# Kernel optimization log

Hardware: AMD Instinct MI355X
Metric: run time of the kernel (lower is better)

Reference implementation:

```python
import jax, jax.numpy as jnp
import numpy as np
from jax import lax

B, Hm, Wm, C, HEADS, MLP_H = 16, 56, 56, 256, 4, 1024
N = Hm * Wm
GRID_STRIDE = 4
N_GRID = (Hm // GRID_STRIDE) * (Wm // GRID_STRIDE)  # 196
K_DOWN = N // 4                                      # 784
K_ADA = K_DOWN - N_GRID
H2, W2 = Hm // 2, Wm // 2
POOL = 7


def _token_order():
    # get_loc: grid tokens first, then adaptive tokens
    pos = np.arange(N)
    tmp = pos.reshape(Hm, Wm)
    pos_grid = tmp[GRID_STRIDE // 2::GRID_STRIDE, GRID_STRIDE // 2::GRID_STRIDE].reshape(-1)
    m = np.ones(N, bool)
    m[pos_grid] = False
    return np.concatenate([pos_grid, pos[m]])


def _loc_init():
    y = 2.0 * ((np.arange(Hm) + 0.5) / Hm) - 1.0
    x = 2.0 * ((np.arange(Wm) + 0.5) / Wm) - 1.0
    xm, ym = np.meshgrid(x, y)
    return np.stack([xm, ym], -1).reshape(-1, 2).astype(np.float32)


_ORDER = _token_order()
_LOC = _loc_init()[_ORDER]


def _ln(x, g, b, eps=1e-5):
    m = jnp.mean(x, -1, keepdims=True)
    v = jnp.mean((x - m) ** 2, -1, keepdims=True)
    return (x - m) * lax.rsqrt(v + eps) * g + b


def _gauss_kernel(ks=3, sigma=2.0):
    c = np.arange(ks, dtype=np.float32)
    xg = np.tile(c, ks).reshape(ks, ks)
    yg = xg.T
    mean = (ks - 1) / 2.0
    var = sigma ** 2
    k = np.exp(-((xg - mean) ** 2 + (yg - mean) ** 2) / (2 * var)) / (2 * np.pi * var)
    return (k / k.sum()).astype(np.float32)


def _gauss_filt(x):
    ch = x.shape[1]
    w = jnp.broadcast_to(jnp.asarray(_gauss_kernel())[None, None], (ch, 1, 3, 3))
    return lax.conv_general_dilated(x, w, (1, 1), [(1, 1), (1, 1)],
                                    feature_group_count=ch,
                                    dimension_numbers=('NCHW', 'OIHW', 'NCHW'))


def _token2map(x, loc, H, W):
    # scatter-add tokens into a [H,W] map, average by count, gaussian hole-fill
    b, n, c = x.shape
    loc = jnp.clip(loc, -1, 1)
    px = jnp.clip(jnp.round(0.5 * (loc[..., 0] + 1) * W - 0.5).astype(jnp.int32), 0, W - 1)
    py = jnp.clip(jnp.round(0.5 * (loc[..., 1] + 1) * H - 0.5).astype(jnp.int32), 0, H - 1)
    idx = (px + py * W + jnp.arange(b)[:, None] * H * W).reshape(-1)
    src = jnp.concatenate([x, jnp.ones((b, n, 1), x.dtype)], -1).reshape(b * n, c + 1)
    out = jnp.zeros((b * H * W, c + 1), x.dtype).at[idx].add(src)
    out = out.reshape(b, H, W, c + 1).transpose(0, 3, 1, 2)
    feat, mask = out[:, :c], out[:, c:]
    feat = feat / (mask + 1e-6)
    mask = (mask > 0).astype(x.dtype)
    feat = feat * mask
    # reconstruct_feature (kernel_size=3, sigma=2)
    fm = _gauss_filt(jnp.concatenate([feat, mask], 1))
    fi = fm[:, :c] / (fm[:, c:] + 1e-6)
    mi = (fm[:, c:] > 0).astype(x.dtype)
    fi = fi * mi
    return feat + (1 - mask) * fi


def _map2token(fm, loc):
    # bilinear grid_sample, align_corners=False, zeros padding
    b, c, H, W = fm.shape
    x = (loc[..., 0] + 1) * 0.5 * W - 0.5
    y = (loc[..., 1] + 1) * 0.5 * H - 0.5
    x0 = jnp.floor(x)
    y0 = jnp.floor(y)
    wx = x - x0
    wy = y - y0
    fm_flat = fm.reshape(b, c, H * W)

    def gather(xi, yi):
        valid = ((xi >= 0) & (xi < W) & (yi >= 0) & (yi < H)).astype(fm.dtype)
        ii = (jnp.clip(yi, 0, H - 1) * W + jnp.clip(xi, 0, W - 1)).astype(jnp.int32)
        v = jnp.take_along_axis(fm_flat, ii[:, None, :], axis=2)  # [b,c,k]
        return v * valid[:, None, :]

    x0i = x0.astype(jnp.int32)
    y0i = y0.astype(jnp.int32)
    v00 = gather(x0i, y0i)
    v01 = gather(x0i + 1, y0i)
    v10 = gather(x0i, y0i + 1)
    v11 = gather(x0i + 1, y0i + 1)
    wx = wx[:, None, :]
    wy = wy[:, None, :]
    out = (v00 * (1 - wx) * (1 - wy) + v01 * wx * (1 - wy)
           + v10 * (1 - wx) * wy + v11 * wx * wy)
    return out.transpose(0, 2, 1)  # [b,k,c]


def _forward(x, ln1_g, ln1_b, wq, wkv, wproj, bproj, sr_w, sr_b, srn_g, srn_b,
             ln2_g, ln2_b, fc1_w, fc1_b, dw_w, dw_b, fc2_w, fc2_b, conf_w, conf_b):
    order = jnp.asarray(_ORDER)
    x = jnp.take(x, order, axis=1)                       # get_loc reorder
    loc = jnp.broadcast_to(jnp.asarray(_LOC)[None], (B, N, 2))
    d = C // HEADS
    # ---- PVT attention (spatial-reduction via 7x7 adaptive pool + 1x1 conv)
    xn = _ln(x, ln1_g, ln1_b)
    q = (xn @ wq).reshape(B, N, HEADS, d).transpose(0, 2, 1, 3)
    fmap = xn.transpose(0, 2, 1).reshape(B, C, Hm, Wm)
    pooled = fmap.reshape(B, C, POOL, Hm // POOL, POOL, Wm // POOL).mean((3, 5))
    sr = jnp.einsum('bihw,oi->bohw', pooled, sr_w) + sr_b[None, :, None, None]
    t = sr.reshape(B, C, POOL * POOL).transpose(0, 2, 1)
    t = jax.nn.gelu(_ln(t, srn_g, srn_b), approximate=False)
    kv = (t @ wkv).reshape(B, POOL * POOL, 2, HEADS, d)
    k = kv[:, :, 0].transpose(0, 2, 1, 3)
    v = kv[:, :, 1].transpose(0, 2, 1, 3)
    a = jax.nn.softmax(jnp.einsum('bhnd,bhmd->bhnm', q, k) * (d ** -0.5), axis=-1)
    o = jnp.einsum('bhnm,bhmd->bhnd', a, v).transpose(0, 2, 1, 3).reshape(B, N, C)
    x = x + o @ wproj + bproj
    # ---- MLP with depthwise conv
    xn = _ln(x, ln2_g, ln2_b)
    h = jax.nn.relu(xn @ fc1_w + fc1_b)
    hm = h.transpose(0, 2, 1).reshape(B, MLP_H, Hm, Wm)
    hm = lax.conv_general_dilated(hm, dw_w, (1, 1), [(1, 1), (1, 1)],
                                  feature_group_count=MLP_H,
                                  dimension_numbers=('NCHW', 'OIHW', 'NCHW'))
    hm = hm + dw_b[None, :, None, None]
    h = jax.nn.gelu(hm.reshape(B, MLP_H, N).transpose(0, 2, 1), approximate=False)
    x = x + h @ fc2_w + fc2_b
    # ---- gumbel top-k selection among adaptive tokens (grid tokens kept)
    conf = (x @ conf_w + conf_b)[..., 0]                 # [B,N]
    u = jax.random.uniform(jax.random.key(1), (B, N - N_GRID), x.dtype)
    g = -jnp.log(-jnp.log(u + 1e-6) + 1e-6)
    scores = conf[:, N_GRID:] + g                        # T=1
    _, idx = lax.top_k(scores, K_ADA)
    x_ada = jnp.take_along_axis(x[:, N_GRID:], idx[..., None], axis=1)
    loc_ada = jnp.take_along_axis(loc[:, N_GRID:], idx[..., None], axis=1)
    x_down = jnp.concatenate([x[:, :N_GRID], x_ada], 1)      # [B,784,C]
    loc_down = jnp.concatenate([loc[:, :N_GRID], loc_ada], 1)
    # ---- token2map (scatter-add + gaussian fill) then map2token (grid sample)
    fmap2 = _token2map(x, loc, H2, W2)
    tok = _map2token(fmap2, loc_down)
    return x_down + tok


def setup_inputs() -> dict:
    key = jax.random.key(0)
    ks = jax.random.split(key, 10)
    s = 0.02

    def rn(k, shape):
        return jax.random.normal(k, shape, jnp.float32) * s

    return {
        'x': jax.random.normal(ks[0], (B, N, C), jnp.float32),
        'ln1_g': jnp.ones((C,), jnp.float32), 'ln1_b': jnp.zeros((C,), jnp.float32),
        'wq': rn(ks[1], (C, C)), 'wkv': rn(ks[2], (C, 2 * C)),
        'wproj': rn(ks[3], (C, C)), 'bproj': jnp.zeros((C,), jnp.float32),
        'sr_w': rn(ks[4], (C, C)), 'sr_b': jnp.zeros((C,), jnp.float32),
        'srn_g': jnp.ones((C,), jnp.float32), 'srn_b': jnp.zeros((C,), jnp.float32),
        'ln2_g': jnp.ones((C,), jnp.float32), 'ln2_b': jnp.zeros((C,), jnp.float32),
        'fc1_w': rn(ks[5], (C, MLP_H)), 'fc1_b': jnp.zeros((MLP_H,), jnp.float32),
        'dw_w': rn(ks[6], (MLP_H, 1, 3, 3)), 'dw_b': jnp.zeros((MLP_H,), jnp.float32),
        'fc2_w': rn(ks[7], (MLP_H, C)), 'fc2_b': jnp.zeros((C,), jnp.float32),
        'conf_w': rn(ks[8], (C, 1)), 'conf_b': jnp.zeros((1,), jnp.float32),
    }


def reference(x, ln1_g, ln1_b, wq, wkv, wproj, bproj, sr_w, sr_b, srn_g, srn_b,
              ln2_g, ln2_b, fc1_w, fc1_b, dw_w, dw_b, fc2_w, fc2_b, conf_w, conf_b):
    return _forward(x, ln1_g, ln1_b, wq, wkv, wproj, bproj, sr_w, sr_b, srn_g, srn_b,
                    ln2_g, ln2_b, fc1_w, fc1_b, dw_w, dw_b, fc2_w, fc2_b, conf_w, conf_b)
```

## Files before the change

### kernel.cpp

```cpp
#include <hip/hip_runtime.h>
#include <math.h>


#define BB 16
#define NN 3136
#define CC 256
#define NHEADS 4
#define DH 64
#define MLPH 1024
#define NGRID 196
#define NREST 2940
#define KADA 588
#define HW 56
#define BCH 2

__device__ __forceinline__ int inv_order(int p) {
  int r = p / HW, c = p % HW;
  if ((r & 3) == 2 && (c & 3) == 2) return (r >> 2) * 14 + (c >> 2);
  int g = ((r + 1) >> 2) * 14 + (((r & 3) == 2) ? ((c + 1) >> 2) : 0);
  return NGRID + p - g;
}

__device__ __forceinline__ double gelu_d(double v) {
  return 0.5 * v * (1.0 + erf(v * 0.70710678118654752440));
}

__device__ __forceinline__ void tf2x32k(unsigned k0, unsigned k1, unsigned x0, unsigned x1,
                                        unsigned& o0, unsigned& o1) {
  unsigned ks[3] = {k0, k1, k0 ^ k1 ^ 0x1BD11BDAu};
  x0 += ks[0]; x1 += ks[1];
  const int rot[2][4] = {{13,15,26,6},{17,29,16,24}};
  #pragma unroll
  for (int i = 0; i < 5; ++i) {
    #pragma unroll
    for (int j = 0; j < 4; ++j) {
      int rr = rot[i & 1][j];
      x0 += x1;
      x1 = (x1 << rr) | (x1 >> (32 - rr));
      x1 ^= x0;
    }
    x0 += ks[(i + 1) % 3];
    x1 += ks[(i + 2) % 3] + (unsigned)(i + 1);
  }
  o0 = x0; o1 = x1;
}

__device__ bool tf_kat() {
  unsigned a, b;
  tf2x32k(0u, 0u, 0u, 0u, a, b);
  if (a != 0x6b200159u || b != 0x99ba4efeu) return false;
  tf2x32k(0xffffffffu, 0xffffffffu, 0xffffffffu, 0xffffffffu, a, b);
  if (a != 0x1cb996fcu || b != 0xbb002be7u) return false;
  tf2x32k(0x13198a2eu, 0x03707344u, 0x243f6a88u, 0x85a308d3u, a, b);
  if (a != 0xc4923a9cu || b != 0x483df7a0u) return false;
  return true;
}

__device__ __forceinline__ double gumbel_d(int f) {
  unsigned o0, o1;
  tf2x32k(0u, 1u, 0u, (unsigned)f, o0, o1);
  unsigned bits = o0 ^ o1;
  float u = __uint_as_float((bits >> 9) | 0x3f800000u) - 1.0f;
  double ud = (double)u;
  return -log(-log(ud + 1e-6) + 1e-6);
}

__global__ void k_order(int* __restrict__ ord) {
  int p = blockIdx.x * 256 + threadIdx.x;
  if (p < NN) ord[inv_order(p)] = p;
}

__global__ __launch_bounds__(256) void k_ln1(const float* __restrict__ x,
    const float* __restrict__ g, const float* __restrict__ b2,
    float* __restrict__ x_r, float* __restrict__ xn) {
  int b = blockIdx.x / NN, p = blockIdx.x % NN;
  int t = threadIdx.x;
  __shared__ double red[256];
  float v = x[((size_t)b*NN + p)*CC + t];
  double vd = (double)v;
  red[t] = vd; __syncthreads();
  for (int s = 128; s > 0; s >>= 1) { if (t < s) red[t] += red[t+s]; __syncthreads(); }
  double m = red[0] * (1.0/CC);
  __syncthreads();
  double d = vd - m;
  red[t] = d*d; __syncthreads();
  for (int s = 128; s > 0; s >>= 1) { if (t < s) red[t] += red[t+s]; __syncthreads(); }
  double var = red[0] * (1.0/CC);
  double o = d * (1.0 / sqrt(var + 1e-5)) * (double)g[t] + (double)b2[t];
  int n = inv_order(p);
  size_t dst = ((size_t)b*NN + n)*CC + t;
  x_r[dst] = v;
  xn[dst] = (float)o;
}

__global__ __launch_bounds__(256) void k_ln2(const float* __restrict__ xin,
    const float* __restrict__ g, const float* __restrict__ b2, float* __restrict__ xo) {
  int row = blockIdx.x;
  int t = threadIdx.x;
  __shared__ double red[256];
  double v = (double)xin[(size_t)row*CC + t];
  red[t] = v; __syncthreads();
  for (int s = 128; s > 0; s >>= 1) { if (t < s) red[t] += red[t+s]; __syncthreads(); }
  double m = red[0] * (1.0/CC);
  __syncthreads();
  double d = v - m;
  red[t] = d*d; __syncthreads();
  for (int s = 128; s > 0; s >>= 1) { if (t < s) red[t] += red[t+s]; __syncthreads(); }
  double var = red[0] * (1.0/CC);
  xo[(size_t)row*CC + t] = (float)(d * (1.0 / sqrt(var + 1e-5)) * (double)g[t] + (double)b2[t]);
}

__global__ __launch_bounds__(256) void k_sr(const float* __restrict__ xn,
    const float* __restrict__ sr_w, const float* __restrict__ sr_b, float* __restrict__ srout) {
  int b = blockIdx.x / 49, cell = blockIdx.x % 49;
  int p1 = cell / 7, p2 = cell % 7;
  int t = threadIdx.x;
  __shared__ double pl[256];
  double s = 0.0;
  #pragma unroll
  for (int i = 0; i < 8; ++i)
    #pragma unroll
    for (int j = 0; j < 8; ++j) {
      int n = (p1*8 + i)*HW + (p2*8 + j);
      s += (double)xn[((size_t)b*NN + n)*CC + t];
    }
  pl[t] = s * (1.0/64.0);
  __syncthreads();
  double acc = (double)sr_b[t];
  for (int i = 0; i < CC; ++i) acc += pl[i] * (double)sr_w[t*CC + i];
  srout[((size_t)b*49 + cell)*CC + t] = (float)acc;
}

__global__ __launch_bounds__(256) void k_kv(const float* __restrict__ srout,
    const float* __restrict__ g, const float* __restrict__ b2,
    const float* __restrict__ wkv, float* __restrict__ kb, float* __restrict__ vb) {
  int b = blockIdx.x / 49, m = blockIdx.x % 49;
  int t = threadIdx.x;
  __shared__ double red[256];
  __shared__ double tl[256];
  double v = (double)srout[((size_t)b*49 + m)*CC + t];
  red[t] = v; __syncthreads();
  for (int s = 128; s > 0; s >>= 1) { if (t < s) red[t] += red[t+s]; __syncthreads(); }
  double mean = red[0] * (1.0/CC);
  __syncthreads();
  double d = v - mean;
  red[t] = d*d; __syncthreads();
  for (int s = 128; s > 0; s >>= 1) { if (t < s) red[t] += red[t+s]; __syncthreads(); }
  double var = red[0] * (1.0/CC);
  double o = d * (1.0 / sqrt(var + 1e-5)) * (double)g[t] + (double)b2[t];
  tl[t] = gelu_d(o);
  __syncthreads();
  #pragma unroll
  for (int rep = 0; rep < 2; ++rep) {
    int j = t + rep*256;
    double acc = 0.0;
    for (int i = 0; i < CC; ++i) acc += tl[i] * (double)wkv[(size_t)i*512 + j];
    int h = (j >> 6) & 3, dd = j & 63;
    float* dst = (j >> 8) ? vb : kb;
    dst[(((size_t)b*NHEADS + h)*49 + m)*DH + dd] = (float)acc;
  }
}

template<int BIAS, int RELU, int RESID>
__global__ __launch_bounds__(256) void k_gemm64(const float* __restrict__ A,
    const float* __restrict__ Bw, const float* __restrict__ bias,
    const float* resid, float* Co, int M, int N, int K) {
  __shared__ __align__(16) float As[16][68];
  __shared__ __align__(16) float Bs[16][68];
  int tid = threadIdx.x;
  int n0 = blockIdx.x * 64, m0 = blockIdx.y * 64;
  int tx = tid & 15, ty = tid >> 4;
  int aM = tid >> 2, aK = (tid & 3) * 4;
  int bK = tid >> 4, bN = (tid & 15) * 4;
  double acc[4][4] = {};
  for (int k0 = 0; k0 < K; k0 += 16) {
    float4 a4 = *(const float4*)&A[(size_t)(m0 + aM) * K + k0 + aK];
    As[aK+0][aM] = a4.x; As[aK+1][aM] = a4.y; As[aK+2][aM] = a4.z; As[aK+3][aM] = a4.w;
    float4 b4 = *(const float4*)&Bw[(size_t)(k0 + bK) * N + n0 + bN];
    *(float4*)&Bs[bK][bN] = b4;
    __syncthreads();
    #pragma unroll
    for (int k = 0; k < 16; ++k) {
      double av[4], bv[4];
      #pragma unroll
      for (int r = 0; r < 4; ++r) av[r] = (double)As[k][ty*4 + r];
      #pragma unroll
      for (int c = 0; c < 4; ++c) bv[c] = (double)Bs[k][tx*4 + c];
      #pragma unroll
      for (int r = 0; r < 4; ++r)
        #pragma unroll
        for (int c = 0; c < 4; ++c)
          acc[r][c] = fma(av[r], bv[c], acc[r][c]);
    }
    __syncthreads();
  }
  #pragma unroll
  for (int r = 0; r < 4; ++r) {
    size_t off = (size_t)(m0 + ty*4 + r) * N + n0 + tx*4;
    #pragma unroll
    for (int c = 0; c < 4; ++c) {
      double v = acc[r][c];
      if (BIAS)  v += (double)bias[n0 + tx*4 + c];
      if (RESID) v += (double)resid[off + c];
      if (RELU)  v = fmax(v, 0.0);
      Co[off + c] = (float)v;
    }
  }
}

__global__ __launch_bounds__(64) void k_attn(float* __restrict__ q,
    const float* __restrict__ kb, const float* __restrict__ vb) {
  int b = blockIdx.x / NN, n = blockIdx.x % NN;
  int t = threadIdx.x;
  __shared__ float qs[256];
  __shared__ double lg[4][52];
  __shared__ double sinv[4];
  float* qrow = q + ((size_t)b*NN + n)*CC;
  #pragma unroll
  for (int i = 0; i < 4; ++i) qs[t + i*64] = qrow[t + i*64];
  __syncthreads();
  for (int li = t; li < 196; li += 64) {
    int h = li / 49, m = li % 49;
    const float* kr = kb + (((size_t)b*NHEADS + h)*49 + m)*DH;
    const float* qh = qs + h*DH;
    double acc = 0.0;
    #pragma unroll 16
    for (int d = 0; d < DH; ++d) acc = fma((double)qh[d], (double)kr[d], acc);
    lg[h][m] = acc * 0.125;
  }
  __syncthreads();
  if (t < 4) {
    double mx = -1e300;
    for (int j = 0; j < 49; ++j) mx = fmax(mx, lg[t][j]);
    double s = 0.0;
    for (int j = 0; j < 49; ++j) { double e = exp(lg[t][j] - mx); lg[t][j] = e; s += e; }
    sinv[t] = 1.0 / s;
  }
  __syncthreads();
  #pragma unroll
  for (int h = 0; h < 4; ++h) {
    const float* vr = vb + (((size_t)b*NHEADS + h)*49)*DH + t;
    double acc = 0.0;
    for (int m = 0; m < 49; ++m) acc = fma(lg[h][m], (double)vr[m*DH], acc);
    qrow[h*64 + t] = (float)(acc * sinv[h]);
  }
}

__global__ __launch_bounds__(256) void k_dw(const float* __restrict__ hb,
    const float* __restrict__ w, const float* __restrict__ bias, float* __restrict__ h2) {
  int bl = blockIdx.x / NN, n = blockIdx.x % NN;
  int r = n / HW, c = n % HW;
  int t = threadIdx.x;
  const size_t base = (size_t)bl * NN;
  #pragma unroll
  for (int it = 0; it < 4; ++it) {
    int mc = t + it*256;
    double acc = (double)bias[mc];
    #pragma unroll
    for (int ky = 0; ky < 3; ++ky) {
      int rr = r + ky - 1;
      if (rr < 0 || rr >= HW) continue;
      #pragma unroll
      for (int kx = 0; kx < 3; ++kx) {
        int cc2 = c + kx - 1;
        if (cc2 < 0 || cc2 >= HW) continue;
        acc = fma((double)w[mc*9 + ky*3 + kx], (double)hb[(base + rr*HW + cc2)*MLPH + mc], acc);
      }
    }
    h2[(base + n)*MLPH + mc] = (float)gelu_d(acc);
  }
}

__global__ __launch_bounds__(1024) void k_topk(const float* __restrict__ x3,
    const float* __restrict__ cw, const float* __restrict__ cb, int* __restrict__ sel) {
  int b = blockIdx.x, t = threadIdx.x;
  __shared__ float wsm[256];
  __shared__ double sc[NREST];
  if (t < 256) wsm[t] = cw[t];
  __syncthreads();
  for (int i = t; i < NREST; i += 1024) {
    const float* xr = x3 + ((size_t)b*NN + NGRID + i)*CC;
    double acc = (double)cb[0];
    #pragma unroll 8
    for (int c = 0; c < CC; ++c) acc += (double)xr[c] * (double)wsm[c];
    sc[i] = acc + gumbel_d(b*NREST + i);
  }
  __syncthreads();
  for (int i = t; i < NREST; i += 1024) {
    double si = sc[i];
    int rank = 0;
    for (int j = 0; j < NREST; ++j) {
      double sj = sc[j];
      rank += (int)((sj > si) | ((sj == si) & (j < i)));
    }
    if (rank < KADA) sel[b*KADA + rank] = NGRID + i;
  }
}

__global__ __launch_bounds__(256) void k_t2m(const float* __restrict__ x3, float* __restrict__ fm) {
  int b = blockIdx.x / 784, pix = blockIdx.x % 784;
  int py = pix / 28, px = pix % 28;
  int t = threadIdx.x;
  float s = 0.f;
  #pragma unroll
  for (int dy = 0; dy < 2; ++dy)
    #pragma unroll
    for (int dx = 0; dx < 2; ++dx) {
      int p = (2*py + dy)*HW + 2*px + dx;
      s += x3[((size_t)b*NN + inv_order(p))*CC + t];
    }
  fm[((size_t)b*784 + pix)*CC + t] = s * (1.0f / 4.000001f);
}

__global__ __launch_bounds__(256) void k_out(const float* __restrict__ x3,
    const float* __restrict__ fm, const int* __restrict__ sel,
    const int* __restrict__ ord, float* __restrict__ out) {
  int b = blockIdx.x / 784, slot = blockIdx.x % 784;
  int t = threadIdx.x;
  int n = (slot < NGRID) ? slot : sel[b*KADA + slot - NGRID];
  int p = ord[n];
  int r = p / HW, c = p % HW;
  int ix0 = (c - 1) >> 1;
  int iy0 = (r - 1) >> 1;
  float wx = (c & 1) ? 0.25f : 0.75f;
  float wy = (r & 1) ? 0.25f : 0.75f;
  const float* fb = fm + (size_t)b*784*CC + t;
  float v = 0.f;
  float w00 = (1.f-wx)*(1.f-wy), w01 = wx*(1.f-wy), w10 = (1.f-wx)*wy, w11 = wx*wy;
  if (ix0 >= 0   && iy0 >= 0)   v += w00 * fb[(iy0*28 + ix0)*CC];
  if (ix0+1 < 28 && iy0 >= 0)   v += w01 * fb[(iy0*28 + ix0+1)*CC];
  if (ix0 >= 0   && iy0+1 < 28) v += w10 * fb[((iy0+1)*28 + ix0)*CC];
  if (ix0+1 < 28 && iy0+1 < 28) v += w11 * fb[((iy0+1)*28 + ix0+1)*CC];
  float res = x3[((size_t)b*NN + n)*CC + t] + v;
  if (blockIdx.x == 0 && t == 0) {
    if (!tf_kat()) res += 1000.0f;
  }
  out[((size_t)b*784 + slot)*CC + t] = res;
}

extern "C" void kernel_launch(void* const* d_in, const int* in_sizes, int n_in,
                              void* d_out, int out_size, void* d_ws, size_t ws_size,
                              hipStream_t stream) {
  const float* x      = (const float*)d_in[0];
  const float* ln1_g  = (const float*)d_in[1];
  const float* ln1_b  = (const float*)d_in[2];
  const float* wq     = (const float*)d_in[3];
  const float* wkv    = (const float*)d_in[4];
  const float* wproj  = (const float*)d_in[5];
  const float* bproj  = (const float*)d_in[6];
  const float* sr_w   = (const float*)d_in[7];
  const float* sr_b   = (const float*)d_in[8];
  const float* srn_g  = (const float*)d_in[9];
  const float* srn_b  = (const float*)d_in[10];
  const float* ln2_g  = (const float*)d_in[11];
  const float* ln2_b  = (const float*)d_in[12];
  const float* fc1_w  = (const float*)d_in[13];
  const float* fc1_b  = (const float*)d_in[14];
  const float* dw_w   = (const float*)d_in[15];
  const float* dw_b   = (const float*)d_in[16];
  const float* fc2_w  = (const float*)d_in[17];
  const float* fc2_b  = (const float*)d_in[18];
  const float* conf_w = (const float*)d_in[19];
  const float* conf_b = (const float*)d_in[20];
  float* out = (float*)d_out;

  float* ws = (float*)d_ws;
  const size_t SZ_XN = (size_t)BB*NN*CC;
  const size_t SZ_H  = (size_t)BCH*NN*MLPH;
  float* x_r   = ws;
  float* xn    = x_r + SZ_XN;
  float* qbuf  = xn + SZ_XN;
  float* hb    = qbuf + SZ_XN;
  float* h2b   = hb + SZ_H;
  float* srout = h2b + SZ_H;
  float* kb    = srout + (size_t)BB*49*CC;
  float* vb    = kb + (size_t)BB*NHEADS*49*DH;
  float* fm    = vb + (size_t)BB*NHEADS*49*DH;
  int*   sel   = (int*)(fm + (size_t)BB*784*CC);
  int*   ord   = sel + BB*KADA;

  k_order<<<(NN+255)/256, 256, 0, stream>>>(ord);
  k_ln1<<<BB*NN, 256, 0, stream>>>(x, ln1_g, ln1_b, x_r, xn);
  k_sr<<<BB*49, 256, 0, stream>>>(xn, sr_w, sr_b, srout);
  k_kv<<<BB*49, 256, 0, stream>>>(srout, srn_g, srn_b, wkv, kb, vb);
  k_gemm64<0,0,0><<<dim3(CC/64, BB*NN/64), 256, 0, stream>>>(xn, wq, nullptr, nullptr, qbuf, BB*NN, CC, CC);
  k_attn<<<BB*NN, 64, 0, stream>>>(qbuf, kb, vb);
  k_gemm64<1,0,1><<<dim3(CC/64, BB*NN/64), 256, 0, stream>>>(qbuf, wproj, bproj, x_r, x_r, BB*NN, CC, CC);
  k_ln2<<<BB*NN, 256, 0, stream>>>(x_r, ln2_g, ln2_b, xn);
  for (int bc = 0; bc < BB/BCH; ++bc) {
    const size_t ro = (size_t)bc * BCH * NN;
    k_gemm64<1,1,0><<<dim3(MLPH/64, BCH*NN/64), 256, 0, stream>>>(xn + ro*CC, fc1_w, fc1_b, nullptr, hb, BCH*NN, MLPH, CC);
    k_dw<<<BCH*NN, 256, 0, stream>>>(hb, dw_w, dw_b, h2b);
    k_gemm64<1,0,1><<<dim3(CC/64, BCH*NN/64), 256, 0, stream>>>(h2b, fc2_w, fc2_b, x_r + ro*CC, x_r + ro*CC, BCH*NN, CC, MLPH);
  }
  k_topk<<<BB, 1024, 0, stream>>>(x_r, conf_w, conf_b, sel);
  k_t2m<<<BB*784, 256, 0, stream>>>(x_r, fm);
  k_out<<<BB*784, 256, 0, stream>>>(x_r, fm, sel, ord, out);
}
```

Before: 3.859 ms.

## Use wave-shuffle LayerNorm reductions, 128-row GEMM tiles, and split top-k into parallel kernels

Replaces the shared-memory tree reductions in the three LayerNorm kernels with 64-lane shuffle reductions and a four-slot combine, cutting barriers. Adds a 128x64 GEMM variant with 8x4 per-thread outputs for the Q, projection and fc1 GEMMs, keeping the 64x64 kernel for fc2. Splits the top-k into a wave-per-token confidence kernel and a ranking kernel spread across 6 blocks per batch, where the old version ran only 16 blocks. Larger GEMM tiles raise register pressure and halve the block count, and the shuffle reductions sum in a different order, so low-order bits can change.

```diff
diff --git a/kernel.cpp b/kernel.cpp
--- a/kernel.cpp
+++ b/kernel.cpp
@@ -75,38 +75,48 @@
     float* __restrict__ x_r, float* __restrict__ xn) {
   int b = blockIdx.x / NN, p = blockIdx.x % NN;
   int t = threadIdx.x;
-  __shared__ double red[256];
+  __shared__ double la[4], lb[4];
   float v = x[((size_t)b*NN + p)*CC + t];
   double vd = (double)v;
-  red[t] = vd; __syncthreads();
-  for (int s = 128; s > 0; s >>= 1) { if (t < s) red[t] += red[t+s]; __syncthreads(); }
-  double m = red[0] * (1.0/CC);
-  __syncthreads();
+  double s = vd;
+  #pragma unroll
+  for (int o = 32; o; o >>= 1) s += __shfl_xor(s, o, 64);
+  if ((t & 63) == 0) la[t >> 6] = s;
+  __syncthreads();
+  double m = (la[0] + la[1] + la[2] + la[3]) * (1.0/CC);
   double d = vd - m;
-  red[t] = d*d; __syncthreads();
-  for (int s = 128; s > 0; s >>= 1) { if (t < s) red[t] += red[t+s]; __syncthreads(); }
-  double var = red[0] * (1.0/CC);
-  double o = d * (1.0 / sqrt(var + 1e-5)) * (double)g[t] + (double)b2[t];
+  s = d * d;
+  #pragma unroll
+  for (int o = 32; o; o >>= 1) s += __shfl_xor(s, o, 64);
+  if ((t & 63) == 0) lb[t >> 6] = s;
+  __syncthreads();
+  double var = (lb[0] + lb[1] + lb[2] + lb[3]) * (1.0/CC);
+  double o2 = d * (1.0 / sqrt(var + 1e-5)) * (double)g[t] + (double)b2[t];
   int n = inv_order(p);
   size_t dst = ((size_t)b*NN + n)*CC + t;
   x_r[dst] = v;
-  xn[dst] = (float)o;
+  xn[dst] = (float)o2;
 }
 
 __global__ __launch_bounds__(256) void k_ln2(const float* __restrict__ xin,
     const float* __restrict__ g, const float* __restrict__ b2, float* __restrict__ xo) {
   int row = blockIdx.x;
   int t = threadIdx.x;
-  __shared__ double red[256];
+  __shared__ double la[4], lb[4];
   double v = (double)xin[(size_t)row*CC + t];
-  red[t] = v; __syncthreads();
-  for (int s = 128; s > 0; s >>= 1) { if (t < s) red[t] += red[t+s]; __syncthreads(); }
-  double m = red[0] * (1.0/CC);
-  __syncthreads();
+  double s = v;
+  #pragma unroll
+  for (int o = 32; o; o >>= 1) s += __shfl_xor(s, o, 64);
+  if ((t & 63) == 0) la[t >> 6] = s;
+  __syncthreads();
+  double m = (la[0] + la[1] + la[2] + la[3]) * (1.0/CC);
   double d = v - m;
-  red[t] = d*d; __syncthreads();
-  for (int s = 128; s > 0; s >>= 1) { if (t < s) red[t] += red[t+s]; __syncthreads(); }
-  double var = red[0] * (1.0/CC);
+  s = d * d;
+  #pragma unroll
+  for (int o = 32; o; o >>= 1) s += __shfl_xor(s, o, 64);
+  if ((t & 63) == 0) lb[t >> 6] = s;
+  __syncthreads();
+  double var = (lb[0] + lb[1] + lb[2] + lb[3]) * (1.0/CC);
   xo[(size_t)row*CC + t] = (float)(d * (1.0 / sqrt(var + 1e-5)) * (double)g[t] + (double)b2[t]);
 }
 
@@ -136,19 +146,24 @@
     const float* __restrict__ wkv, float* __restrict__ kb, float* __restrict__ vb) {
   int b = blockIdx.x / 49, m = blockIdx.x % 49;
   int t = threadIdx.x;
-  __shared__ double red[256];
+  __shared__ double la[4], lb[4];
   __shared__ double tl[256];
   double v = (double)srout[((size_t)b*49 + m)*CC + t];
-  red[t] = v; __syncthreads();
-  for (int s = 128; s > 0; s >>= 1) { if (t < s) red[t] += red[t+s]; __syncthreads(); }
-  double mean = red[0] * (1.0/CC);
-  __syncthreads();
+  double s = v;
+  #pragma unroll
+  for (int o = 32; o; o >>= 1) s += __shfl_xor(s, o, 64);
+  if ((t & 63) == 0) la[t >> 6] = s;
+  __syncthreads();
+  double mean = (la[0] + la[1] + la[2] + la[3]) * (1.0/CC);
   double d = v - mean;
-  red[t] = d*d; __syncthreads();
-  for (int s = 128; s > 0; s >>= 1) { if (t < s) red[t] += red[t+s]; __syncthreads(); }
-  double var = red[0] * (1.0/CC);
-  double o = d * (1.0 / sqrt(var + 1e-5)) * (double)g[t] + (double)b2[t];
-  tl[t] = gelu_d(o);
+  s = d * d;
+  #pragma unroll
+  for (int o = 32; o; o >>= 1) s += __shfl_xor(s, o, 64);
+  if ((t & 63) == 0) lb[t >> 6] = s;
+  __syncthreads();
+  double var = (lb[0] + lb[1] + lb[2] + lb[3]) * (1.0/CC);
+  double o2 = d * (1.0 / sqrt(var + 1e-5)) * (double)g[t] + (double)b2[t];
+  tl[t] = gelu_d(o2);
   __syncthreads();
   #pragma unroll
   for (int rep = 0; rep < 2; ++rep) {
@@ -162,7 +177,58 @@
 }
 
 template<int BIAS, int RELU, int RESID>
-__global__ __launch_bounds__(256) void k_gemm64(const float* __restrict__ A,
+__global__ __launch_bounds__(256) void k_gemmA(const float* __restrict__ A,
+    const float* __restrict__ Bw, const float* __restrict__ bias,
+    const float* resid, float* Co, int M, int N, int K) {
+  __shared__ __align__(16) float As[16][132];
+  __shared__ __align__(16) float Bs[16][68];
+  int tid = threadIdx.x;
+  int n0 = blockIdx.x * 64, m0 = blockIdx.y * 128;
+  int tx = tid & 15, ty = tid >> 4;
+  int aM = tid >> 2, aK = (tid & 3) * 4;
+  int bK = tid >> 4, bN = (tid & 15) * 4;
+  double acc[8][4] = {};
+  for (int k0 = 0; k0 < K; k0 += 16) {
+    #pragma unroll
+    for (int ps = 0; ps < 2; ++ps) {
+      float4 a4 = *(const float4*)&A[(size_t)(m0 + aM + ps*64) * K + k0 + aK];
+      As[aK+0][aM+ps*64] = a4.x; As[aK+1][aM+ps*64] = a4.y;
+      As[aK+2][aM+ps*64] = a4.z; As[aK+3][aM+ps*64] = a4.w;
+    }
+    float4 b4 = *(const float4*)&Bw[(size_t)(k0 + bK) * N + n0 + bN];
+    *(float4*)&Bs[bK][bN] = b4;
+    __syncthreads();
+    #pragma unroll
+    for (int k = 0; k < 16; ++k) {
+      double av[8], bv[4];
+      #pragma unroll
+      for (int r = 0; r < 8; ++r) av[r] = (double)As[k][ty*8 + r];
+      #pragma unroll
+      for (int c = 0; c < 4; ++c) bv[c] = (double)Bs[k][tx*4 + c];
+      #pragma unroll
+      for (int r = 0; r < 8; ++r)
+        #pragma unroll
+        for (int c = 0; c < 4; ++c)
+          acc[r][c] = fma(av[r], bv[c], acc[r][c]);
+    }
+    __syncthreads();
+  }
+  #pragma unroll
+  for (int r = 0; r < 8; ++r) {
+    size_t off = (size_t)(m0 + ty*8 + r) * N + n0 + tx*4;
+    #pragma unroll
+    for (int c = 0; c < 4; ++c) {
+      double v = acc[r][c];
+      if (BIAS)  v += (double)bias[n0 + tx*4 + c];
+      if (RESID) v += (double)resid[off + c];
+      if (RELU)  v = fmax(v, 0.0);
+      Co[off + c] = (float)v;
+    }
+  }
+}
+
+template<int BIAS, int RELU, int RESID>
+__global__ __launch_bounds__(256) void k_gemmB(const float* __restrict__ A,
     const float* __restrict__ Bw, const float* __restrict__ bias,
     const float* resid, float* Co, int M, int N, int K) {
   __shared__ __align__(16) float As[16][68];
@@ -271,24 +337,33 @@
   }
 }
 
-__global__ __launch_bounds__(1024) void k_topk(const float* __restrict__ x3,
-    const float* __restrict__ cw, const float* __restrict__ cb, int* __restrict__ sel) {
-  int b = blockIdx.x, t = threadIdx.x;
-  __shared__ float wsm[256];
+__global__ __launch_bounds__(256) void k_conf(const float* __restrict__ x3,
+    const float* __restrict__ cw, const float* __restrict__ cb, double* __restrict__ scd) {
+  int wid = (blockIdx.x * 256 + threadIdx.x) >> 6;
+  int lane = threadIdx.x & 63;
+  if (wid >= BB * NREST) return;
+  int b = wid / NREST, i = wid % NREST;
+  const float* xr = x3 + ((size_t)b*NN + NGRID + i)*CC;
+  double acc = 0.0;
+  #pragma unroll
+  for (int r = 0; r < 4; ++r)
+    acc += (double)xr[lane + r*64] * (double)cw[lane + r*64];
+  #pragma unroll
+  for (int o = 32; o; o >>= 1) acc += __shfl_xor(acc, o, 64);
+  if (lane == 0) scd[wid] = acc + (double)cb[0] + gumbel_d(wid);
+}
+
+__global__ __launch_bounds__(512) void k_topk2(const double* __restrict__ scd, int* __restrict__ sel) {
+  int b = blockIdx.x / 6, chunk = blockIdx.x % 6;
   __shared__ double sc[NREST];
-  if (t < 256) wsm[t] = cw[t];
-  __syncthreads();
-  for (int i = t; i < NREST; i += 1024) {
-    const float* xr = x3 + ((size_t)b*NN + NGRID + i)*CC;
-    double acc = (double)cb[0];
-    #pragma unroll 8
-    for (int c = 0; c < CC; ++c) acc += (double)xr[c] * (double)wsm[c];
-    sc[i] = acc + gumbel_d(b*NREST + i);
-  }
-  __syncthreads();
-  for (int i = t; i < NREST; i += 1024) {
+  const double* s = scd + (size_t)b * NREST;
+  for (int j = threadIdx.x; j < NREST; j += 512) sc[j] = s[j];
+  __syncthreads();
+  int i = chunk * 512 + threadIdx.x;
+  if (i < NREST) {
     double si = sc[i];
     int rank = 0;
+    #pragma unroll 8
     for (int j = 0; j < NREST; ++j) {
       double sj = sc[j];
       rank += (int)((sj > si) | ((sj == si) & (j < i)));
@@ -376,24 +451,26 @@
   float* kb    = srout + (size_t)BB*49*CC;
   float* vb    = kb + (size_t)BB*NHEADS*49*DH;
   float* fm    = vb + (size_t)BB*NHEADS*49*DH;
-  int*   sel   = (int*)(fm + (size_t)BB*784*CC);
+  double* scd  = (double*)(fm + (size_t)BB*784*CC);
+  int*   sel   = (int*)(scd + (size_t)BB*NREST);
   int*   ord   = sel + BB*KADA;
 
   k_order<<<(NN+255)/256, 256, 0, stream>>>(ord);
   k_ln1<<<BB*NN, 256, 0, stream>>>(x, ln1_g, ln1_b, x_r, xn);
   k_sr<<<BB*49, 256, 0, stream>>>(xn, sr_w, sr_b, srout);
   k_kv<<<BB*49, 256, 0, stream>>>(srout, srn_g, srn_b, wkv, kb, vb);
-  k_gemm64<0,0,0><<<dim3(CC/64, BB*NN/64), 256, 0, stream>>>(xn, wq, nullptr, nullptr, qbuf, BB*NN, CC, CC);
+  k_gemmA<0,0,0><<<dim3(CC/64, BB*NN/128), 256, 0, stream>>>(xn, wq, nullptr, nullptr, qbuf, BB*NN, CC, CC);
   k_attn<<<BB*NN, 64, 0, stream>>>(qbuf, kb, vb);
-  k_gemm64<1,0,1><<<dim3(CC/64, BB*NN/64), 256, 0, stream>>>(qbuf, wproj, bproj, x_r, x_r, BB*NN, CC, CC);
+  k_gemmA<1,0,1><<<dim3(CC/64, BB*NN/128), 256, 0, stream>>>(qbuf, wproj, bproj, x_r, x_r, BB*NN, CC, CC);
   k_ln2<<<BB*NN, 256, 0, stream>>>(x_r, ln2_g, ln2_b, xn);
   for (int bc = 0; bc < BB/BCH; ++bc) {
     const size_t ro = (size_t)bc * BCH * NN;
-    k_gemm64<1,1,0><<<dim3(MLPH/64, BCH*NN/64), 256, 0, stream>>>(xn + ro*CC, fc1_w, fc1_b, nullptr, hb, BCH*NN, MLPH, CC);
+    k_gemmA<1,1,0><<<dim3(MLPH/64, BCH*NN/128), 256, 0, stream>>>(xn + ro*CC, fc1_w, fc1_b, nullptr, hb, BCH*NN, MLPH, CC);
     k_dw<<<BCH*NN, 256, 0, stream>>>(hb, dw_w, dw_b, h2b);
-    k_gemm64<1,0,1><<<dim3(CC/64, BCH*NN/64), 256, 0, stream>>>(h2b, fc2_w, fc2_b, x_r + ro*CC, x_r + ro*CC, BCH*NN, CC, MLPH);
-  }
-  k_topk<<<BB, 1024, 0, stream>>>(x_r, conf_w, conf_b, sel);
+    k_gemmB<1,0,1><<<dim3(CC/64, BCH*NN/64), 256, 0, stream>>>(h2b, fc2_w, fc2_b, x_r + ro*CC, x_r + ro*CC, BCH*NN, CC, MLPH);
+  }
+  k_conf<<<(BB*NREST*64 + 255)/256, 256, 0, stream>>>(x_r, conf_w, conf_b, scd);
+  k_topk2<<<BB*6, 512, 0, stream>>>(scd, sel);
   k_t2m<<<BB*784, 256, 0, stream>>>(x_r, fm);
   k_out<<<BB*784, 256, 0, stream>>>(x_r, fm, sel, ord, out);
 }
```

After: 3.590 ms. 1.08x faster.
